# Performance work log

Hardware: AMD Instinct MI355X
Metric: run time of the kernel (lower is better)

Reference implementation:

```python
import jax, jax.numpy as jnp
import numpy as np
from jax import lax

B, H, W = 32, 512, 512
NLAND, NF = 100000, 16
EPS = 1e-3  # Keras BatchNormalization default epsilon
DN = ('NHWC', 'HWIO', 'NHWC')


def setup_inputs() -> dict:
    key = jax.random.key(0)
    ks = jax.random.split(key, 7)
    x = jax.random.normal(ks[0], (B, NLAND), dtype=jnp.float32)
    flat_indices = jax.random.randint(ks[1], (NLAND,), 0, H * W, dtype=jnp.int32)
    conv1_w = jax.random.normal(ks[2], (3, 3, 1, NF), dtype=jnp.float32) * 0.1
    conv1_b = jnp.zeros((NF,), jnp.float32)
    gamma = jnp.ones((NF,), jnp.float32)
    beta = jnp.zeros((NF,), jnp.float32)
    moving_mean = jax.random.normal(ks[3], (NF,), dtype=jnp.float32) * 0.1
    moving_var = jax.random.uniform(ks[4], (NF,), dtype=jnp.float32) + 0.5
    # Original inits conv2 to zeros; use small random weights so the op is non-trivial.
    conv2_w = jax.random.normal(ks[5], (3, 3, NF, 1), dtype=jnp.float32) * 0.05
    conv2_b = jnp.zeros((1,), jnp.float32)
    return {"x": x, "conv1_w": conv1_w, "conv1_b": conv1_b, "gamma": gamma,
            "beta": beta, "moving_mean": moving_mean, "moving_var": moving_var,
            "conv2_w": conv2_w, "conv2_b": conv2_b, "flat_indices": flat_indices}


def reference(x, conv1_w, conv1_b, gamma, beta, moving_mean, moving_var,
              conv2_w, conv2_b, flat_indices):
    hw = H * W
    # scatter land values onto flat grid (tf.scatter_nd adds on duplicate indices)
    grid = jnp.zeros((x.shape[0], hw), x.dtype).at[:, flat_indices].add(x)
    g = grid.reshape(-1, H, W, 1)                      # [B,H,W,1]
    y = lax.conv_general_dilated(g, conv1_w, (1, 1), 'SAME', dimension_numbers=DN)
    y = jax.nn.relu(y + conv1_b)                       # Conv2D(relu)
    # BatchNorm in inference mode (training=None)
    y = gamma * (y - moving_mean) * lax.rsqrt(moving_var + EPS) + beta
    y = lax.conv_general_dilated(y, conv2_w, (1, 1), 'SAME', dimension_numbers=DN)
    y = y + conv2_b                                    # [B,H,W,1]
    refined_fl = y.reshape(-1, hw)
    adjustment = refined_fl[:, flat_indices]           # gather land points back
    return x + adjustment
```

## Files before the change

kernel.cpp:

```cpp
#include <hip/hip_runtime.h>
#include <hip/hip_bf16.h>

#define HH 512
#define WW 512
#define HWSZ (HH*WW)
#define NB 32
#define NLD 100000
#define NF 16
#define EPSV 1e-3f
#define TILE 16
#define GR (TILE+4)
#define HCELLS (GR*GR)
#define RDW 10
#define YR (TILE+2)
#define NGRP 21
#define PSLOTS (NGRP*16)
#define PSTRB 10
#define PBUF (PSLOTS*PSTRB)

#define NTILE 1024
#define CAPT 256

typedef __attribute__((ext_vector_type(4))) short bf16x4;
typedef __attribute__((ext_vector_type(4))) float f32x4;

static __device__ __forceinline__ unsigned short f2bfu(float f) {
  __hip_bfloat16 h = __float2bfloat16(f);
  return __builtin_bit_cast(unsigned short, h);
}
static __device__ __forceinline__ unsigned cvtpk(float a, float b) {
  unsigned r;
  asm("v_cvt_pk_bf16_f32 %0, %1, %2" : "=v"(r) : "v"(a), "v"(b));
  return r;
}
static __device__ __forceinline__ f32x4 mfma16(bf16x4 a, bf16x4 b, f32x4 c) {
#if defined(__HIP_DEVICE_COMPILE__)
#if __has_builtin(__builtin_amdgcn_mfma_f32_16x16x16_bf16)
  return __builtin_amdgcn_mfma_f32_16x16x16_bf16(a, b, c, 0, 0, 0);
#else
  return __builtin_amdgcn_mfma_f32_16x16x16bf16_1k(a, b, c, 0, 0, 0);
#endif
#else
  return c;
#endif
}

__global__ __launch_bounds__(256) void bin_k(const int* __restrict__ idx,
    const float* __restrict__ w1g, const float* __restrict__ b1g,
    const float* __restrict__ w2g, const float* __restrict__ gammag,
    const float* __restrict__ betag, const float* __restrict__ mmg,
    const float* __restrict__ mvg,
    uint2* __restrict__ w1A, uint2* __restrict__ w2A, float* __restrict__ g_const,
    unsigned* __restrict__ g_tcnt, unsigned* __restrict__ g_tbkt) {
  __shared__ unsigned ht[NTILE], bt[NTILE];
  const int lid = threadIdx.x;

  if (blockIdx.x == 0 && lid < 64) {
    int m = lid & 15, kg = lid >> 4;
    bf16x4 a1, a2;
    #pragma unroll
    for (int jj = 0; jj < 4; ++jj) {
      int k = kg*4 + jj;
      float v1 = 0.f;
      if (k < 12) {
        int col = k & 3, row = k >> 2;
        if (col < 3) v1 = w1g[(row*3+col)*NF + m];
      } else if (k == 12) v1 = b1g[m];
      a1[jj] = (short)f2bfu(v1);
      float v2 = 0.f;
      if (m < 9) {
        float bnA = gammag[k]*rsqrtf(mvg[k] + EPSV);
        v2 = w2g[m*NF + k]*bnA;
      }
      a2[jj] = (short)f2bfu(v2);
    }
    w1A[lid] = __builtin_bit_cast(uint2, a1);
    w2A[lid] = __builtin_bit_cast(uint2, a2);
  }
  if (blockIdx.x == 0 && lid >= 64 && lid < 64+9) {
    int t = lid - 64;
    float s = 0.f;
    #pragma unroll
    for (int c = 0; c < NF; ++c) {
      float A = gammag[c]*rsqrtf(mvg[c] + EPSV);
      s += w2g[t*NF + c]*(betag[c] - mmg[c]*A);
    }
    g_const[t] = s;
  }

  for (int q = lid; q < NTILE; q += 256) ht[q] = 0;
  __syncthreads();
  for (int i = blockIdx.x*256 + lid; i < NLD; i += 64*256) {
    int cell = idx[i];
    int h = cell >> 9, w = cell & 511;
    int thA = (h-2)>>4, thB = (h+2)>>4;
    int twA = (w-2)>>4, twB = (w+2)>>4;
    #pragma unroll
    for (int ah = 0; ah < 2; ++ah) {
      int th = ah ? thB : thA;
      if (th < 0 || th > 31 || (ah && thB == thA)) continue;
      #pragma unroll
      for (int aw = 0; aw < 2; ++aw) {
        int tw = aw ? twB : twA;
        if (tw < 0 || tw > 31 || (aw && twB == twA)) continue;
        atomicAdd(&ht[th*32 + tw], 1u);
      }
    }
  }
  __syncthreads();
  for (int q = lid; q < NTILE; q += 256) {
    bt[q] = ht[q] ? atomicAdd(&g_tcnt[q], ht[q]) : 0u;
    ht[q] = 0;
  }
  __syncthreads();
  for (int i = blockIdx.x*256 + lid; i < NLD; i += 64*256) {
    int cell = idx[i];
    int h = cell >> 9, w = cell & 511;
    int thA = (h-2)>>4, thB = (h+2)>>4;
    int twA = (w-2)>>4, twB = (w+2)>>4;
    #pragma unroll
    for (int ah = 0; ah < 2; ++ah) {
      int th = ah ? thB : thA;
      if (th < 0 || th > 31 || (ah && thB == thA)) continue;
      #pragma unroll
      for (int aw = 0; aw < 2; ++aw) {
        int tw = aw ? twB : twA;
        if (tw < 0 || tw > 31 || (aw && twB == twA)) continue;
        int t = th*32 + tw;
        unsigned pt = bt[t] + atomicAdd(&ht[t], 1u);
        unsigned pos = (unsigned)(h - th*16 + 2)*20u + (unsigned)(w - tw*16 + 2);
        if (pt < CAPT) g_tbkt[(size_t)t*CAPT + pt] = ((unsigned)i << 9) | pos;
      }
    }
  }
}

__global__ __launch_bounds__(256, 4) void conv_k(
    const uint2* __restrict__ w1Ag, const uint2* __restrict__ w2Ag,
    const float* __restrict__ g_const, const float* __restrict__ b2g,
    const float* __restrict__ x,
    const unsigned* __restrict__ g_tcnt, const unsigned* __restrict__ g_tbkt,
    float* __restrict__ out)
{
  __shared__ float s_gridf[2*HCELLS];
  __shared__ unsigned s_gE[2][GR*RDW];
  __shared__ unsigned s_gO[2][GR*RDW];
  __shared__ __align__(8) unsigned short s_projb[2*PBUF];
  __shared__ float s_const[12];

  const int lid = threadIdx.x;
  const int j = blockIdx.x;
  const int b0 = (j & 15) * 2;
  const int tile = j >> 4;
  const int ty0 = (tile >> 5) * TILE, tx0 = (tile & 31) * TILE;

  const int l = lid & 63;
  const int wid = lid >> 6;
  const bf16x4 w1frag = __builtin_bit_cast(bf16x4, w1Ag[l]);
  const bf16x4 w2frag = __builtin_bit_cast(bf16x4, w2Ag[l]);

  if (lid < 9) s_const[lid] = g_const[lid];
  for (int q = lid; q < 2*HCELLS; q += 256) s_gridf[q] = 0.f;
  __syncthreads();

  const unsigned nT = min(g_tcnt[tile], (unsigned)CAPT);
  const unsigned* tb = g_tbkt + (size_t)tile*CAPT;
  const float* xb0 = x + (size_t)b0*NLD;
  const float* xb1 = xb0 + NLD;
  for (unsigned k2 = lid; k2 < nT; k2 += 256) {
    unsigned e = tb[k2];
    unsigned pos = e & 511, i = e >> 9;
    atomicAdd(&s_gridf[pos],          xb0[i]);
    atomicAdd(&s_gridf[HCELLS + pos], xb1[i]);
  }
  __syncthreads();

  for (int q = lid; q < 2*GR*RDW; q += 256) {
    int bb = q >= GR*RDW;
    int rj = q - bb*GR*RDW;
    int r = rj / RDW, jd = rj - r*RDW;
    const float* f = &s_gridf[bb*HCELLS + r*GR];
    int c0 = jd*2;
    s_gE[bb][rj] = cvtpk(f[c0], f[c0+1]);
    s_gO[bb][rj] = cvtpk(f[c0+1], (c0+2 < GR) ? f[c0+2] : 0.f);
  }
  __syncthreads();

  {
    const int n_px = l & 15, kg = l >> 4;

    for (int grp = wid; grp < NGRP; grp += 4) {
      int p = grp*16 + n_px;
      unsigned rr = ((unsigned)p * 3641u) >> 16;
      unsigned cc = (unsigned)p - rr*18u;
      int yh = ty0 - 1 + (int)rr, yw = tx0 - 1 + (int)cc;
      bool val = ((unsigned)yh < HH) & ((unsigned)yw < WW);
      int o = (int)rr*RDW + (int)(cc >> 1) + kg*RDW;
      const unsigned* g0 = (cc & 1) ? s_gO[0] : s_gE[0];
      const unsigned* g1 = (cc & 1) ? s_gO[1] : s_gE[1];

      unsigned ga0, ga1, gb0, gb1;
      if (kg < 3) { ga0 = g0[o]; ga1 = g0[o+1]; gb0 = g1[o]; gb1 = g1[o+1]; }
      else        { ga0 = 0x00003F80u; ga1 = 0u; gb0 = 0x00003F80u; gb1 = 0u; }
      bf16x4 gf0 = __builtin_bit_cast(bf16x4, make_uint2(ga0, ga1));
      bf16x4 gf1 = __builtin_bit_cast(bf16x4, make_uint2(gb0, gb1));

      f32x4 z = {0.f,0.f,0.f,0.f};
      f32x4 d10 = mfma16(w1frag, gf0, z);
      f32x4 d11 = mfma16(w1frag, gf1, z);

      unsigned u0a = cvtpk(fmaxf(d10[0],0.f), fmaxf(d10[1],0.f));
      unsigned u0b = cvtpk(fmaxf(d10[2],0.f), fmaxf(d10[3],0.f));
      unsigned u1a = cvtpk(fmaxf(d11[0],0.f), fmaxf(d11[1],0.f));
      unsigned u1b = cvtpk(fmaxf(d11[2],0.f), fmaxf(d11[3],0.f));
      if (!val) { u0a = u0b = u1a = u1b = 0u; }
      bf16x4 bf0 = __builtin_bit_cast(bf16x4, make_uint2(u0a, u0b));
      bf16x4 bf1 = __builtin_bit_cast(bf16x4, make_uint2(u1a, u1b));

      f32x4 d0 = mfma16(w2frag, bf0, z);
      f32x4 d1 = mfma16(w2frag, bf1, z);

      if (kg < 2) {
        *(uint2*)&s_projb[p*PSTRB + kg*4]        = make_uint2(cvtpk(d0[0],d0[1]), cvtpk(d0[2],d0[3]));
        *(uint2*)&s_projb[PBUF + p*PSTRB + kg*4] = make_uint2(cvtpk(d1[0],d1[1]), cvtpk(d1[2],d1[3]));
      } else if (kg == 2) {
        s_projb[p*PSTRB + 8]        = (unsigned short)(cvtpk(d0[0], d0[0]) & 0xFFFFu);
        s_projb[PBUF + p*PSTRB + 8] = (unsigned short)(cvtpk(d1[0], d1[0]) & 0xFFFFu);
      }
    }
  }
  __syncthreads();

  float* s_ytile = s_gridf;
  {
    const int ty = lid >> 4, tx = lid & 15;
    bool vh[3], vw[3];
    #pragma unroll
    for (int kk = 0; kk < 3; ++kk) {
      vh[kk] = (unsigned)(ty0 + ty + kk - 1) < HH;
      vw[kk] = (unsigned)(tx0 + tx + kk - 1) < WW;
    }
    float base = b2g[0];
    float acc0 = 0.f, acc1 = 0.f;
    #pragma unroll
    for (int kh = 0; kh < 3; ++kh)
      #pragma unroll
      for (int kw = 0; kw < 3; ++kw) {
        if (vh[kh] & vw[kw]) base += s_const[kh*3+kw];
        int o = ((ty+kh)*YR + tx+kw)*PSTRB + kh*3+kw;
        acc0 += __uint_as_float((unsigned)s_projb[o] << 16);
        acc1 += __uint_as_float((unsigned)s_projb[PBUF + o] << 16);
      }
    s_ytile[lid]       = base + acc0;
    s_ytile[256 + lid] = base + acc1;
  }
  __syncthreads();

  for (unsigned k2 = lid; k2 < nT; k2 += 256) {
    unsigned e = tb[k2];
    unsigned pos = e & 511;
    unsigned py = (pos * 3277u) >> 16;
    unsigned px2 = pos - py*20u;
    if (py >= 2 && py < 18 && px2 >= 2 && px2 < 18) {
      unsigned i = e >> 9;
      int o = (int)((py-2)*16 + (px2-2));
      out[(size_t)b0*NLD + i]     = xb0[i] + s_ytile[o];
      out[(size_t)(b0+1)*NLD + i] = xb1[i] + s_ytile[256 + o];
    }
  }
}

extern "C" void kernel_launch(void* const* d_in, const int* in_sizes, int n_in,
                              void* d_out, int out_size, void* d_ws, size_t ws_size,
                              hipStream_t stream) {
  const float* x     = (const float*)d_in[0];
  const float* w1    = (const float*)d_in[1];
  const float* b1    = (const float*)d_in[2];
  const float* gamma = (const float*)d_in[3];
  const float* beta  = (const float*)d_in[4];
  const float* mmean = (const float*)d_in[5];
  const float* mvar  = (const float*)d_in[6];
  const float* w2    = (const float*)d_in[7];
  const float* b2    = (const float*)d_in[8];
  const int*   idx   = (const int*)d_in[9];
  float* out = (float*)d_out;

  unsigned* g_tcnt = (unsigned*)d_ws;
  unsigned* g_tbkt = g_tcnt + NTILE;
  uint2*    w1A    = (uint2*)(g_tbkt + (size_t)NTILE*CAPT);
  uint2*    w2A    = w1A + 64;
  float*    gconst = (float*)(w2A + 64);

  (void)hipMemsetAsync(g_tcnt, 0, NTILE*sizeof(unsigned), stream);

  bin_k<<<dim3(64), dim3(256), 0, stream>>>(idx, w1, b1, w2, gamma, beta,
                                            mmean, mvar, w1A, w2A, gconst,
                                            g_tcnt, g_tbkt);

  conv_k<<<dim3((NB/2) * NTILE), dim3(256), 0, stream>>>(
      w1A, w2A, gconst, b2, x, g_tcnt, g_tbkt, out);
}
```

Measured before the change: 91.18 us.

## Process eight tiles per block and prefetch next tile's bucket and x values

Each block now loops over eight consecutive tiles instead of one, which cuts the grid size by a factor of eight. The next tile's bucket entries and x values are loaded into registers during the current tile's compute so global-load latency overlaps with the conv work. The x values are kept in registers and reused for the final output write instead of being reloaded. In exchange there are fewer blocks to spread across CUs, an extra barrier per tile, and lid < nT assumes CAPT is at most 256.

```diff
diff --git a/kernel.cpp b/kernel.cpp
--- a/kernel.cpp
+++ b/kernel.cpp
@@ -20,6 +20,7 @@
 
 #define NTILE 1024
 #define CAPT 256
+#define TPB 8
 
 typedef __attribute__((ext_vector_type(4))) short bf16x4;
 typedef __attribute__((ext_vector_type(4))) float f32x4;
@@ -151,122 +152,150 @@
   const int lid = threadIdx.x;
   const int j = blockIdx.x;
   const int b0 = (j & 15) * 2;
-  const int tile = j >> 4;
-  const int ty0 = (tile >> 5) * TILE, tx0 = (tile & 31) * TILE;
-
+  const int seq = j >> 4;
   const int l = lid & 63;
   const int wid = lid >> 6;
   const bf16x4 w1frag = __builtin_bit_cast(bf16x4, w1Ag[l]);
   const bf16x4 w2frag = __builtin_bit_cast(bf16x4, w2Ag[l]);
-
-  if (lid < 9) s_const[lid] = g_const[lid];
-  for (int q = lid; q < 2*HCELLS; q += 256) s_gridf[q] = 0.f;
-  __syncthreads();
-
-  const unsigned nT = min(g_tcnt[tile], (unsigned)CAPT);
-  const unsigned* tb = g_tbkt + (size_t)tile*CAPT;
+  const float b2v = b2g[0];
+
   const float* xb0 = x + (size_t)b0*NLD;
   const float* xb1 = xb0 + NLD;
-  for (unsigned k2 = lid; k2 < nT; k2 += 256) {
-    unsigned e = tb[k2];
-    unsigned pos = e & 511, i = e >> 9;
-    atomicAdd(&s_gridf[pos],          xb0[i]);
-    atomicAdd(&s_gridf[HCELLS + pos], xb1[i]);
-  }
-  __syncthreads();
-
-  for (int q = lid; q < 2*GR*RDW; q += 256) {
-    int bb = q >= GR*RDW;
-    int rj = q - bb*GR*RDW;
-    int r = rj / RDW, jd = rj - r*RDW;
-    const float* f = &s_gridf[bb*HCELLS + r*GR];
-    int c0 = jd*2;
-    s_gE[bb][rj] = cvtpk(f[c0], f[c0+1]);
-    s_gO[bb][rj] = cvtpk(f[c0+1], (c0+2 < GR) ? f[c0+2] : 0.f);
-  }
-  __syncthreads();
-
+
+  if (lid < 9) s_const[lid] = g_const[lid];
+
+  int tile = seq * TPB;
+  bool valid;
+  unsigned e = 0; float xv0 = 0.f, xv1 = 0.f;
   {
-    const int n_px = l & 15, kg = l >> 4;
-
-    for (int grp = wid; grp < NGRP; grp += 4) {
-      int p = grp*16 + n_px;
-      unsigned rr = ((unsigned)p * 3641u) >> 16;
-      unsigned cc = (unsigned)p - rr*18u;
-      int yh = ty0 - 1 + (int)rr, yw = tx0 - 1 + (int)cc;
-      bool val = ((unsigned)yh < HH) & ((unsigned)yw < WW);
-      int o = (int)rr*RDW + (int)(cc >> 1) + kg*RDW;
-      const unsigned* g0 = (cc & 1) ? s_gO[0] : s_gE[0];
-      const unsigned* g1 = (cc & 1) ? s_gO[1] : s_gE[1];
-
-      unsigned ga0, ga1, gb0, gb1;
-      if (kg < 3) { ga0 = g0[o]; ga1 = g0[o+1]; gb0 = g1[o]; gb1 = g1[o+1]; }
-      else        { ga0 = 0x00003F80u; ga1 = 0u; gb0 = 0x00003F80u; gb1 = 0u; }
-      bf16x4 gf0 = __builtin_bit_cast(bf16x4, make_uint2(ga0, ga1));
-      bf16x4 gf1 = __builtin_bit_cast(bf16x4, make_uint2(gb0, gb1));
-
-      f32x4 z = {0.f,0.f,0.f,0.f};
-      f32x4 d10 = mfma16(w1frag, gf0, z);
-      f32x4 d11 = mfma16(w1frag, gf1, z);
-
-      unsigned u0a = cvtpk(fmaxf(d10[0],0.f), fmaxf(d10[1],0.f));
-      unsigned u0b = cvtpk(fmaxf(d10[2],0.f), fmaxf(d10[3],0.f));
-      unsigned u1a = cvtpk(fmaxf(d11[0],0.f), fmaxf(d11[1],0.f));
-      unsigned u1b = cvtpk(fmaxf(d11[2],0.f), fmaxf(d11[3],0.f));
-      if (!val) { u0a = u0b = u1a = u1b = 0u; }
-      bf16x4 bf0 = __builtin_bit_cast(bf16x4, make_uint2(u0a, u0b));
-      bf16x4 bf1 = __builtin_bit_cast(bf16x4, make_uint2(u1a, u1b));
-
-      f32x4 d0 = mfma16(w2frag, bf0, z);
-      f32x4 d1 = mfma16(w2frag, bf1, z);
-
-      if (kg < 2) {
-        *(uint2*)&s_projb[p*PSTRB + kg*4]        = make_uint2(cvtpk(d0[0],d0[1]), cvtpk(d0[2],d0[3]));
-        *(uint2*)&s_projb[PBUF + p*PSTRB + kg*4] = make_uint2(cvtpk(d1[0],d1[1]), cvtpk(d1[2],d1[3]));
-      } else if (kg == 2) {
-        s_projb[p*PSTRB + 8]        = (unsigned short)(cvtpk(d0[0], d0[0]) & 0xFFFFu);
-        s_projb[PBUF + p*PSTRB + 8] = (unsigned short)(cvtpk(d1[0], d1[0]) & 0xFFFFu);
-      }
-    }
-  }
-  __syncthreads();
-
-  float* s_ytile = s_gridf;
-  {
-    const int ty = lid >> 4, tx = lid & 15;
-    bool vh[3], vw[3];
-    #pragma unroll
-    for (int kk = 0; kk < 3; ++kk) {
-      vh[kk] = (unsigned)(ty0 + ty + kk - 1) < HH;
-      vw[kk] = (unsigned)(tx0 + tx + kk - 1) < WW;
-    }
-    float base = b2g[0];
-    float acc0 = 0.f, acc1 = 0.f;
-    #pragma unroll
-    for (int kh = 0; kh < 3; ++kh)
+    unsigned nT = min(g_tcnt[tile], (unsigned)CAPT);
+    valid = (unsigned)lid < nT;
+    if (valid) {
+      e = g_tbkt[(size_t)tile*CAPT + lid];
+      xv0 = xb0[e >> 9];
+      xv1 = xb1[e >> 9];
+    }
+  }
+
+  for (int s = 0; s < TPB; ++s, ++tile) {
+    const int ty0 = (tile >> 5) * TILE, tx0 = (tile & 31) * TILE;
+
+    for (int q = lid; q < 2*HCELLS; q += 256) s_gridf[q] = 0.f;
+    __syncthreads();
+
+    if (valid) {
+      unsigned pos = e & 511;
+      atomicAdd(&s_gridf[pos],          xv0);
+      atomicAdd(&s_gridf[HCELLS + pos], xv1);
+    }
+    __syncthreads();
+
+    for (int q = lid; q < 2*GR*RDW; q += 256) {
+      int bb = q >= GR*RDW;
+      int rj = q - bb*GR*RDW;
+      int r = rj / RDW, jd = rj - r*RDW;
+      const float* f = &s_gridf[bb*HCELLS + r*GR];
+      int c0 = jd*2;
+      s_gE[bb][rj] = cvtpk(f[c0], f[c0+1]);
+      s_gO[bb][rj] = cvtpk(f[c0+1], (c0+2 < GR) ? f[c0+2] : 0.f);
+    }
+
+    bool valid_n = false;
+    unsigned e_n = 0; float xn0 = 0.f, xn1 = 0.f;
+    if (s < TPB-1) {
+      unsigned nT_n = min(g_tcnt[tile+1], (unsigned)CAPT);
+      valid_n = (unsigned)lid < nT_n;
+      if (valid_n) {
+        e_n = g_tbkt[(size_t)(tile+1)*CAPT + lid];
+        xn0 = xb0[e_n >> 9];
+        xn1 = xb1[e_n >> 9];
+      }
+    }
+    __syncthreads();
+
+    {
+      const int n_px = l & 15, kg = l >> 4;
+      for (int grp = wid; grp < NGRP; grp += 4) {
+        int p = grp*16 + n_px;
+        unsigned rr = ((unsigned)p * 3641u) >> 16;
+        unsigned cc = (unsigned)p - rr*18u;
+        int yh = ty0 - 1 + (int)rr, yw = tx0 - 1 + (int)cc;
+        bool val = ((unsigned)yh < HH) & ((unsigned)yw < WW);
+        int o = (int)rr*RDW + (int)(cc >> 1) + kg*RDW;
+        const unsigned* g0 = (cc & 1) ? s_gO[0] : s_gE[0];
+        const unsigned* g1 = (cc & 1) ? s_gO[1] : s_gE[1];
+
+        unsigned ga0, ga1, gb0, gb1;
+        if (kg < 3) { ga0 = g0[o]; ga1 = g0[o+1]; gb0 = g1[o]; gb1 = g1[o+1]; }
+        else        { ga0 = 0x00003F80u; ga1 = 0u; gb0 = 0x00003F80u; gb1 = 0u; }
+        bf16x4 gf0 = __builtin_bit_cast(bf16x4, make_uint2(ga0, ga1));
+        bf16x4 gf1 = __builtin_bit_cast(bf16x4, make_uint2(gb0, gb1));
+
+        f32x4 z = {0.f,0.f,0.f,0.f};
+        f32x4 d10 = mfma16(w1frag, gf0, z);
+        f32x4 d11 = mfma16(w1frag, gf1, z);
+
+        unsigned u0a = cvtpk(fmaxf(d10[0],0.f), fmaxf(d10[1],0.f));
+        unsigned u0b = cvtpk(fmaxf(d10[2],0.f), fmaxf(d10[3],0.f));
+        unsigned u1a = cvtpk(fmaxf(d11[0],0.f), fmaxf(d11[1],0.f));
+        unsigned u1b = cvtpk(fmaxf(d11[2],0.f), fmaxf(d11[3],0.f));
+        if (!val) { u0a = u0b = u1a = u1b = 0u; }
+        bf16x4 bf0 = __builtin_bit_cast(bf16x4, make_uint2(u0a, u0b));
+        bf16x4 bf1 = __builtin_bit_cast(bf16x4, make_uint2(u1a, u1b));
+
+        f32x4 d0 = mfma16(w2frag, bf0, z);
+        f32x4 d1 = mfma16(w2frag, bf1, z);
+
+        if (kg < 2) {
+          *(uint2*)&s_projb[p*PSTRB + kg*4]        = make_uint2(cvtpk(d0[0],d0[1]), cvtpk(d0[2],d0[3]));
+          *(uint2*)&s_projb[PBUF + p*PSTRB + kg*4] = make_uint2(cvtpk(d1[0],d1[1]), cvtpk(d1[2],d1[3]));
+        } else if (kg == 2) {
+          s_projb[p*PSTRB + 8]        = (unsigned short)(cvtpk(d0[0], d0[0]) & 0xFFFFu);
+          s_projb[PBUF + p*PSTRB + 8] = (unsigned short)(cvtpk(d1[0], d1[0]) & 0xFFFFu);
+        }
+      }
+    }
+    __syncthreads();
+
+    float* s_ytile = s_gridf;
+    {
+      const int ty = lid >> 4, tx = lid & 15;
+      bool vh[3], vw[3];
       #pragma unroll
-      for (int kw = 0; kw < 3; ++kw) {
-        if (vh[kh] & vw[kw]) base += s_const[kh*3+kw];
-        int o = ((ty+kh)*YR + tx+kw)*PSTRB + kh*3+kw;
-        acc0 += __uint_as_float((unsigned)s_projb[o] << 16);
-        acc1 += __uint_as_float((unsigned)s_projb[PBUF + o] << 16);
-      }
-    s_ytile[lid]       = base + acc0;
-    s_ytile[256 + lid] = base + acc1;
-  }
-  __syncthreads();
-
-  for (unsigned k2 = lid; k2 < nT; k2 += 256) {
-    unsigned e = tb[k2];
-    unsigned pos = e & 511;
-    unsigned py = (pos * 3277u) >> 16;
-    unsigned px2 = pos - py*20u;
-    if (py >= 2 && py < 18 && px2 >= 2 && px2 < 18) {
-      unsigned i = e >> 9;
-      int o = (int)((py-2)*16 + (px2-2));
-      out[(size_t)b0*NLD + i]     = xb0[i] + s_ytile[o];
-      out[(size_t)(b0+1)*NLD + i] = xb1[i] + s_ytile[256 + o];
-    }
+      for (int kk = 0; kk < 3; ++kk) {
+        vh[kk] = (unsigned)(ty0 + ty + kk - 1) < HH;
+        vw[kk] = (unsigned)(tx0 + tx + kk - 1) < WW;
+      }
+      float base = b2v;
+      float acc0 = 0.f, acc1 = 0.f;
+      #pragma unroll
+      for (int kh = 0; kh < 3; ++kh)
+        #pragma unroll
+        for (int kw = 0; kw < 3; ++kw) {
+          if (vh[kh] & vw[kw]) base += s_const[kh*3+kw];
+          int o = ((ty+kh)*YR + tx+kw)*PSTRB + kh*3+kw;
+          acc0 += __uint_as_float((unsigned)s_projb[o] << 16);
+          acc1 += __uint_as_float((unsigned)s_projb[PBUF + o] << 16);
+        }
+      s_ytile[lid]       = base + acc0;
+      s_ytile[256 + lid] = base + acc1;
+    }
+    __syncthreads();
+
+    if (valid) {
+      unsigned pos = e & 511;
+      unsigned py = (pos * 3277u) >> 16;
+      unsigned px2 = pos - py*20u;
+      if (py >= 2 && py < 18 && px2 >= 2 && px2 < 18) {
+        unsigned i = e >> 9;
+        int o = (int)((py-2)*16 + (px2-2));
+        out[(size_t)b0*NLD + i]     = xv0 + s_ytile[o];
+        out[(size_t)(b0+1)*NLD + i] = xv1 + s_ytile[256 + o];
+      }
+    }
+
+    e = e_n; xv0 = xn0; xv1 = xn1; valid = valid_n;
+    __syncthreads();
   }
 }
 
@@ -297,6 +326,6 @@
                                             mmean, mvar, w1A, w2A, gconst,
                                             g_tcnt, g_tbkt);
 
-  conv_k<<<dim3((NB/2) * NTILE), dim3(256), 0, stream>>>(
+  conv_k<<<dim3((NB/2) * (NTILE/TPB)), dim3(256), 0, stream>>>(
       w1A, w2A, gconst, b2, x, g_tcnt, g_tbkt, out);
 }
```

Result: slower. 100.2 us (+9.9%).
